# Kernel optimization log

Hardware: AMD Instinct MI355X
Metric: run time of the kernel (lower is better)

Reference implementation:

```python
import jax, jax.numpy as jnp
import numpy as np

N = 8192
D_IN = 512
D_OUT = 128
DENSITY = 0.004  # avg degree ~32
NEG_INF = -1.0e10
LEAKY_ALPHA = 0.2  # tf.nn.leaky_relu default


def setup_inputs() -> dict:
    key = jax.random.key(0)
    k_x, k_adj, k_w, k_as, k_an = jax.random.split(key, 5)
    x = jax.random.normal(k_x, (N, D_IN), dtype=jnp.float32)
    # sparse binary adjacency, materialized dense (as the module does via tf.sparse.to_dense)
    adj = (jax.random.uniform(k_adj, (N, N)) < DENSITY).astype(jnp.float32)
    adj = jnp.maximum(adj, jnp.eye(N, dtype=jnp.float32))  # self-loops so softmax rows are valid
    W = jax.random.normal(k_w, (D_IN, D_OUT), dtype=jnp.float32) * (1.0 / np.sqrt(D_IN))
    attn_self = jax.random.normal(k_as, (D_OUT, 1), dtype=jnp.float32) * 0.1
    attn_neigh = jax.random.normal(k_an, (D_OUT, 1), dtype=jnp.float32) * 0.1
    return {"x": x, "adj": adj, "W": W, "attn_self": attn_self, "attn_neigh": attn_neigh}


def reference(x, adj, W, attn_self, attn_neigh):
    # dropouts are 0.0 -> identity
    h = x @ W                                   # [N, D_OUT]
    a_s = h @ attn_self                          # [N, 1]
    a_n = h @ attn_neigh                         # [N, 1]
    e = a_s + a_n.T                              # [N, N] additive attention logits
    e = jnp.where(e >= 0, e, LEAKY_ALPHA * e)    # leaky_relu
    e = e + NEG_INF * (1.0 - adj)                # mask non-edges
    attn = jax.nn.softmax(e, axis=-1)            # row-wise softmax [N, N]
    out = attn @ h                               # [N, D_OUT]
    return jax.nn.relu(out)
```

## Files before the change

### kernel.cpp

```cpp
#include <hip/hip_runtime.h>
#include <hip/hip_bf16.h>
#include <cstdint>

#define NN 8192
#define DIN 512
#define DOUT 128
#define NEG_SLOPE 0.2f
#define MAXE 256
#define GEMM_BLOCKS 1024

typedef float fvec4 __attribute__((ext_vector_type(4)));

__device__ inline fvec4 ntload4(const float* p) {
    return __builtin_nontemporal_load((const fvec4*)p);
}

__global__ __launch_bounds__(256) void k_fused(
    const float* __restrict__ x, const float* __restrict__ W,
    const float* __restrict__ attn_self, const float* __restrict__ attn_neigh,
    const float* __restrict__ adj,
    float* __restrict__ h, float* __restrict__ a_s, float* __restrict__ a_n,
    int* __restrict__ e_cnt, int* __restrict__ e_idx) {
    __shared__ char smem_raw[16384];
    __shared__ int s_cnt;
    const int tid = threadIdx.x;
    const int bid = blockIdx.x;

    if (bid < GEMM_BLOCKS) {
        float4* xs = (float4*)smem_raw;
        const int m0 = bid * 8;
        const float4* x4 = (const float4*)(x + (size_t)m0 * DIN);
#pragma unroll
        for (int r = 0; r < 4; ++r) xs[tid + 256 * r] = x4[tid + 256 * r];
        __syncthreads();

        const int c4 = tid & 31;
        const int rg = tid >> 5;
        const float4* W4 = (const float4*)W;
        const float4* xr = xs + rg * 128;
        float4 acc = {0.f, 0.f, 0.f, 0.f};
#pragma unroll 4
        for (int k4 = 0; k4 < 128; ++k4) {
            float4 xv = xr[k4];
            float4 w0 = W4[(4 * k4 + 0) * 32 + c4];
            float4 w1 = W4[(4 * k4 + 1) * 32 + c4];
            float4 w2 = W4[(4 * k4 + 2) * 32 + c4];
            float4 w3 = W4[(4 * k4 + 3) * 32 + c4];
            acc.x += xv.x * w0.x + xv.y * w1.x + xv.z * w2.x + xv.w * w3.x;
            acc.y += xv.x * w0.y + xv.y * w1.y + xv.z * w2.y + xv.w * w3.y;
            acc.z += xv.x * w0.z + xv.y * w1.z + xv.z * w2.z + xv.w * w3.z;
            acc.w += xv.x * w0.w + xv.y * w1.w + xv.z * w2.w + xv.w * w3.w;
        }
        const int row = m0 + rg;
        ((float4*)h)[(size_t)row * 32 + c4] = acc;

        float4 as4 = ((const float4*)attn_self)[c4];
        float4 an4 = ((const float4*)attn_neigh)[c4];
        float ps = acc.x * as4.x + acc.y * as4.y + acc.z * as4.z + acc.w * as4.w;
        float pn = acc.x * an4.x + acc.y * an4.y + acc.z * an4.z + acc.w * an4.w;
#pragma unroll
        for (int off = 16; off > 0; off >>= 1) {
            ps += __shfl_xor(ps, off);
            pn += __shfl_xor(pn, off);
        }
        if (c4 == 0) { a_s[row] = ps; a_n[row] = pn; }
    } else {
        const int i = bid - GEMM_BLOCKS;
        int* s_idx = (int*)smem_raw;
        if (tid == 0) s_cnt = 0;
        __syncthreads();

        const float* arow = adj + ((size_t)i << 13);
        fvec4 v[8];
#pragma unroll
        for (int r = 0; r < 8; ++r) v[r] = ntload4(arow + 4 * (tid + 256 * r));
#pragma unroll
        for (int r = 0; r < 8; ++r) {
            int base = (tid + 256 * r) * 4;
#pragma unroll
            for (int q = 0; q < 4; ++q) {
                if (v[r][q] != 0.f) {
                    int p = atomicAdd(&s_cnt, 1);
                    if (p < MAXE) s_idx[p] = base + q;
                }
            }
        }
        __syncthreads();
        const int cnt = min(s_cnt, MAXE);
        for (int t = tid; t < cnt; t += 256) e_idx[(size_t)i * MAXE + t] = s_idx[t];
        if (tid == 0) e_cnt[i] = cnt;
    }
}

__global__ __launch_bounds__(256) void k_soft(
    const float* __restrict__ h, const float* __restrict__ a_s,
    const float* __restrict__ a_n, const int* __restrict__ e_cnt,
    const int* __restrict__ e_idx, float* __restrict__ out) {
    const int tid = threadIdx.x;
    const int lane = tid & 63;
    const int i = blockIdx.x * 4 + (tid >> 6);
    const int cnt = e_cnt[i];
    const float asi = a_s[i];

    float acc0 = 0.f, acc1 = 0.f, lsum = 0.f;
    for (int base = 0; base < cnt; base += 64) {
        const int len = min(64, cnt - base);
        int j = 0; float w = 0.f;
        if (lane < len) {
            j = e_idx[(size_t)i * MAXE + base + lane];
            float e = asi + a_n[j];
            e = (e >= 0.f) ? e : NEG_SLOPE * e;
            w = __expf(e);
        }
        lsum += w;
        int t = 0;
        for (; t + 1 < len; t += 2) {
            int jj0 = __shfl(j, t);     float ww0 = __shfl(w, t);
            int jj1 = __shfl(j, t + 1); float ww1 = __shfl(w, t + 1);
            float h00 = h[(size_t)jj0 * DOUT + lane];
            float h01 = h[(size_t)jj0 * DOUT + 64 + lane];
            float h10 = h[(size_t)jj1 * DOUT + lane];
            float h11 = h[(size_t)jj1 * DOUT + 64 + lane];
            acc0 += ww0 * h00 + ww1 * h10;
            acc1 += ww0 * h01 + ww1 * h11;
        }
        if (t < len) {
            int jj = __shfl(j, t); float ww = __shfl(w, t);
            acc0 += ww * h[(size_t)jj * DOUT + lane];
            acc1 += ww * h[(size_t)jj * DOUT + 64 + lane];
        }
    }
#pragma unroll
    for (int off = 32; off > 0; off >>= 1) lsum += __shfl_xor(lsum, off);
    const float inv_d = 1.0f / lsum;
    out[(size_t)i * DOUT + lane]      = fmaxf(acc0 * inv_d, 0.f);
    out[(size_t)i * DOUT + 64 + lane] = fmaxf(acc1 * inv_d, 0.f);
}

extern "C" void kernel_launch(void* const* d_in, const int* in_sizes, int n_in,
                              void* d_out, int out_size, void* d_ws, size_t ws_size,
                              hipStream_t stream) {
    const float* x          = (const float*)d_in[0];
    const float* adj        = (const float*)d_in[1];
    const float* W          = (const float*)d_in[2];
    const float* attn_self  = (const float*)d_in[3];
    const float* attn_neigh = (const float*)d_in[4];
    float* out = (float*)d_out;

    float* h   = (float*)d_ws;
    float* a_s = h + (size_t)NN * DOUT;
    float* a_n = a_s + NN;
    int* e_cnt = (int*)(a_n + NN);
    int* e_idx = e_cnt + NN;

    hipLaunchKernelGGL(k_fused, dim3(GEMM_BLOCKS + NN), dim3(256), 0, stream,
                       x, W, attn_self, attn_neigh, adj, h, a_s, a_n, e_cnt, e_idx);
    hipLaunchKernelGGL(k_soft, dim3(NN / 4), dim3(256), 0, stream,
                       h, a_s, a_n, e_cnt, e_idx, out);
}
```

Before: 410.7 us.

## Fuse adjacency scan with softmax aggregation into per-row kernel, split GEMM out

Moves the adjacency row compaction into the same kernel that computes attention weights and aggregates neighbor features, keeping edge indices in shared memory instead of writing and rereading them from global memory. The GEMM that produces h and the attention scalars now runs as its own kernel before the row kernel. This removes the edge-list round trip but gives up the overlap between the GEMM and the adjacency scan that the previous combined launch had.

Measured after the change: 420.9 us. 1.02x slower.

```diff
diff --git a/kernel.cpp b/kernel.cpp
--- a/kernel.cpp
+++ b/kernel.cpp
@@ -1,5 +1,4 @@
 #include <hip/hip_runtime.h>
-#include <hip/hip_bf16.h>
 #include <cstdint>
 
 #define NN 8192
@@ -15,126 +14,118 @@
     return __builtin_nontemporal_load((const fvec4*)p);
 }
 
-__global__ __launch_bounds__(256) void k_fused(
+__global__ __launch_bounds__(256) void k_gemm(
     const float* __restrict__ x, const float* __restrict__ W,
     const float* __restrict__ attn_self, const float* __restrict__ attn_neigh,
-    const float* __restrict__ adj,
-    float* __restrict__ h, float* __restrict__ a_s, float* __restrict__ a_n,
-    int* __restrict__ e_cnt, int* __restrict__ e_idx) {
-    __shared__ char smem_raw[16384];
+    float* __restrict__ h, float* __restrict__ a_s, float* __restrict__ a_n) {
+    __shared__ float4 xs[1024];
+    const int tid = threadIdx.x;
+    const int m0 = blockIdx.x * 8;
+    const float4* x4 = (const float4*)(x + (size_t)m0 * DIN);
+#pragma unroll
+    for (int r = 0; r < 4; ++r) xs[tid + 256 * r] = x4[tid + 256 * r];
+    __syncthreads();
+
+    const int c4 = tid & 31;
+    const int rg = tid >> 5;
+    const float4* W4 = (const float4*)W;
+    const float4* xr = xs + rg * 128;
+    float4 acc = {0.f, 0.f, 0.f, 0.f};
+#pragma unroll 4
+    for (int k4 = 0; k4 < 128; ++k4) {
+        float4 xv = xr[k4];
+        float4 w0 = W4[(4 * k4 + 0) * 32 + c4];
+        float4 w1 = W4[(4 * k4 + 1) * 32 + c4];
+        float4 w2 = W4[(4 * k4 + 2) * 32 + c4];
+        float4 w3 = W4[(4 * k4 + 3) * 32 + c4];
+        acc.x += xv.x * w0.x + xv.y * w1.x + xv.z * w2.x + xv.w * w3.x;
+        acc.y += xv.x * w0.y + xv.y * w1.y + xv.z * w2.y + xv.w * w3.y;
+        acc.z += xv.x * w0.z + xv.y * w1.z + xv.z * w2.z + xv.w * w3.z;
+        acc.w += xv.x * w0.w + xv.y * w1.w + xv.z * w2.w + xv.w * w3.w;
+    }
+    const int row = m0 + rg;
+    ((float4*)h)[(size_t)row * 32 + c4] = acc;
+
+    float4 as4 = ((const float4*)attn_self)[c4];
+    float4 an4 = ((const float4*)attn_neigh)[c4];
+    float ps = acc.x * as4.x + acc.y * as4.y + acc.z * as4.z + acc.w * as4.w;
+    float pn = acc.x * an4.x + acc.y * an4.y + acc.z * an4.z + acc.w * an4.w;
+#pragma unroll
+    for (int off = 16; off > 0; off >>= 1) {
+        ps += __shfl_xor(ps, off);
+        pn += __shfl_xor(pn, off);
+    }
+    if (c4 == 0) { a_s[row] = ps; a_n[row] = pn; }
+}
+
+__global__ __launch_bounds__(256) void k_row(
+    const float* __restrict__ adj, const float* __restrict__ h,
+    const float* __restrict__ a_s, const float* __restrict__ a_n,
+    float* __restrict__ out) {
+    __shared__ int s_idx[MAXE];
+    __shared__ float s_w[MAXE];
+    __shared__ float s_acc[DOUT];
+    __shared__ float s_wp[DOUT];
     __shared__ int s_cnt;
     const int tid = threadIdx.x;
-    const int bid = blockIdx.x;
+    const int i = blockIdx.x;
+    if (tid == 0) s_cnt = 0;
+    __syncthreads();
 
-    if (bid < GEMM_BLOCKS) {
-        float4* xs = (float4*)smem_raw;
-        const int m0 = bid * 8;
-        const float4* x4 = (const float4*)(x + (size_t)m0 * DIN);
+    const float* arow = adj + ((size_t)i << 13);
+    fvec4 v[8];
 #pragma unroll
-        for (int r = 0; r < 4; ++r) xs[tid + 256 * r] = x4[tid + 256 * r];
-        __syncthreads();
-
-        const int c4 = tid & 31;
-        const int rg = tid >> 5;
-        const float4* W4 = (const float4*)W;
-        const float4* xr = xs + rg * 128;
-        float4 acc = {0.f, 0.f, 0.f, 0.f};
-#pragma unroll 4
-        for (int k4 = 0; k4 < 128; ++k4) {
-            float4 xv = xr[k4];
-            float4 w0 = W4[(4 * k4 + 0) * 32 + c4];
-            float4 w1 = W4[(4 * k4 + 1) * 32 + c4];
-            float4 w2 = W4[(4 * k4 + 2) * 32 + c4];
-            float4 w3 = W4[(4 * k4 + 3) * 32 + c4];
-            acc.x += xv.x * w0.x + xv.y * w1.x + xv.z * w2.x + xv.w * w3.x;
-            acc.y += xv.x * w0.y + xv.y * w1.y + xv.z * w2.y + xv.w * w3.y;
-            acc.z += xv.x * w0.z + xv.y * w1.z + xv.z * w2.z + xv.w * w3.z;
-            acc.w += xv.x * w0.w + xv.y * w1.w + xv.z * w2.w + xv.w * w3.w;
-        }
-        const int row = m0 + rg;
-        ((float4*)h)[(size_t)row * 32 + c4] = acc;
-
-        float4 as4 = ((const float4*)attn_self)[c4];
-        float4 an4 = ((const float4*)attn_neigh)[c4];
-        float ps = acc.x * as4.x + acc.y * as4.y + acc.z * as4.z + acc.w * as4.w;
-        float pn = acc.x * an4.x + acc.y * an4.y + acc.z * an4.z + acc.w * an4.w;
+    for (int r = 0; r < 8; ++r) v[r] = ntload4(arow + 4 * (tid + 256 * r));
 #pragma unroll
-        for (int off = 16; off > 0; off >>= 1) {
-            ps += __shfl_xor(ps, off);
-            pn += __shfl_xor(pn, off);
-        }
-        if (c4 == 0) { a_s[row] = ps; a_n[row] = pn; }
-    } else {
-        const int i = bid - GEMM_BLOCKS;
-        int* s_idx = (int*)smem_raw;
-        if (tid == 0) s_cnt = 0;
-        __syncthreads();
-
-        const float* arow = adj + ((size_t)i << 13);
-        fvec4 v[8];
+    for (int r = 0; r < 8; ++r) {
+        int base = (tid + 256 * r) * 4;
 #pragma unroll
-        for (int r = 0; r < 8; ++r) v[r] = ntload4(arow + 4 * (tid + 256 * r));
-#pragma unroll
-        for (int r = 0; r < 8; ++r) {
-            int base = (tid + 256 * r) * 4;
-#pragma unroll
-            for (int q = 0; q < 4; ++q) {
-                if (v[r][q] != 0.f) {
-                    int p = atomicAdd(&s_cnt, 1);
-                    if (p < MAXE) s_idx[p] = base + q;
-                }
+        for (int q = 0; q < 4; ++q) {
+            if (v[r][q] != 0.f) {
+                int p = atomicAdd(&s_cnt, 1);
+                if (p < MAXE) s_idx[p] = base + q;
             }
         }
-        __syncthreads();
-        const int cnt = min(s_cnt, MAXE);
-        for (int t = tid; t < cnt; t += 256) e_idx[(size_t)i * MAXE + t] = s_idx[t];
-        if (tid == 0) e_cnt[i] = cnt;
     }
-}
+    __syncthreads();
+    const int cnt = min(s_cnt, MAXE);
 
-__global__ __launch_bounds__(256) void k_soft(
-    const float* __restrict__ h, const float* __restrict__ a_s,
-    const float* __restrict__ a_n, const int* __restrict__ e_cnt,
-    const int* __restrict__ e_idx, float* __restrict__ out) {
-    const int tid = threadIdx.x;
-    const int lane = tid & 63;
-    const int i = blockIdx.x * 4 + (tid >> 6);
-    const int cnt = e_cnt[i];
     const float asi = a_s[i];
+    if (tid < cnt) {
+        int j = s_idx[tid];
+        float e = asi + a_n[j];
+        e = (e >= 0.f) ? e : NEG_SLOPE * e;
+        s_w[tid] = __expf(e);
+    }
+    __syncthreads();
 
-    float acc0 = 0.f, acc1 = 0.f, lsum = 0.f;
-    for (int base = 0; base < cnt; base += 64) {
-        const int len = min(64, cnt - base);
-        int j = 0; float w = 0.f;
-        if (lane < len) {
-            j = e_idx[(size_t)i * MAXE + base + lane];
-            float e = asi + a_n[j];
-            e = (e >= 0.f) ? e : NEG_SLOPE * e;
-            w = __expf(e);
-        }
-        lsum += w;
-        int t = 0;
-        for (; t + 1 < len; t += 2) {
-            int jj0 = __shfl(j, t);     float ww0 = __shfl(w, t);
-            int jj1 = __shfl(j, t + 1); float ww1 = __shfl(w, t + 1);
-            float h00 = h[(size_t)jj0 * DOUT + lane];
-            float h01 = h[(size_t)jj0 * DOUT + 64 + lane];
-            float h10 = h[(size_t)jj1 * DOUT + lane];
-            float h11 = h[(size_t)jj1 * DOUT + 64 + lane];
-            acc0 += ww0 * h00 + ww1 * h10;
-            acc1 += ww0 * h01 + ww1 * h11;
-        }
-        if (t < len) {
-            int jj = __shfl(j, t); float ww = __shfl(w, t);
-            acc0 += ww * h[(size_t)jj * DOUT + lane];
-            acc1 += ww * h[(size_t)jj * DOUT + 64 + lane];
-        }
+    const int c = tid & 127;
+    const int half = tid >> 7;
+    float acc = 0.f, wp = 0.f;
+    int t = half;
+    for (; t + 2 < cnt; t += 4) {
+        int j0 = s_idx[t];
+        int j1 = s_idx[t + 2];
+        float w0 = s_w[t];
+        float w1 = s_w[t + 2];
+        float h0 = h[(size_t)j0 * DOUT + c];
+        float h1 = h[(size_t)j1 * DOUT + c];
+        acc += w0 * h0 + w1 * h1;
+        wp += w0 + w1;
     }
-#pragma unroll
-    for (int off = 32; off > 0; off >>= 1) lsum += __shfl_xor(lsum, off);
-    const float inv_d = 1.0f / lsum;
-    out[(size_t)i * DOUT + lane]      = fmaxf(acc0 * inv_d, 0.f);
-    out[(size_t)i * DOUT + 64 + lane] = fmaxf(acc1 * inv_d, 0.f);
+    for (; t < cnt; t += 2) {
+        int j = s_idx[t];
+        float w = s_w[t];
+        acc += w * h[(size_t)j * DOUT + c];
+        wp += w;
+    }
+    if (half == 0) { s_acc[c] = acc; s_wp[c] = wp; }
+    __syncthreads();
+    if (half) {
+        float tot = acc + s_acc[c];
+        float wsum = wp + s_wp[c];
+        out[(size_t)i * DOUT + c] = fmaxf(tot * (1.0f / wsum), 0.f);
+    }
 }
 
 extern "C" void kernel_launch(void* const* d_in, const int* in_sizes, int n_in,
@@ -150,11 +141,9 @@
     float* h   = (float*)d_ws;
     float* a_s = h + (size_t)NN * DOUT;
     float* a_n = a_s + NN;
-    int* e_cnt = (int*)(a_n + NN);
-    int* e_idx = e_cnt + NN;
 
-    hipLaunchKernelGGL(k_fused, dim3(GEMM_BLOCKS + NN), dim3(256), 0, stream,
-                       x, W, attn_self, attn_neigh, adj, h, a_s, a_n, e_cnt, e_idx);
-    hipLaunchKernelGGL(k_soft, dim3(NN / 4), dim3(256), 0, stream,
-                       h, a_s, a_n, e_cnt, e_idx, out);
+    hipLaunchKernelGGL(k_gemm, dim3(GEMM_BLOCKS), dim3(256), 0, stream,
+                       x, W, attn_self, attn_neigh, h, a_s, a_n);
+    hipLaunchKernelGGL(k_row, dim3(NN), dim3(256), 0, stream,
+                       adj, h, a_s, a_n, out);
 }
```
